# Performance work log

Hardware: AMD Instinct MI355X
Metric: run time of the kernel (lower is better)

Reference implementation:

```python
import jax, jax.numpy as jnp
import numpy as np

L, D, N_HEADS = 4096, 1024, 16
HEAD_D = D // N_HEADS


def setup_inputs() -> dict:
    key = jax.random.key(0)
    kx, kq, kbq, ko, kbo = jax.random.split(key, 5)
    lim_in = 1.0 / np.sqrt(D)
    return {
        "x": jax.random.normal(kx, (L, D), dtype=jnp.float32),
        # equinox nn.Linear(dim, 3*dim): weight [3D, D], bias [3D], uniform(-1/sqrt(in), 1/sqrt(in))
        "W_qkv": jax.random.uniform(kq, (3 * D, D), jnp.float32, -lim_in, lim_in),
        "b_qkv": jax.random.uniform(kbq, (3 * D,), jnp.float32, -lim_in, lim_in),
        "W_out": jax.random.uniform(ko, (D, D), jnp.float32, -lim_in, lim_in),
        "b_out": jax.random.uniform(kbo, (D,), jnp.float32, -lim_in, lim_in),
    }


def reference(x, W_qkv, b_qkv, W_out, b_out):
    # qkv projection: equinox Linear computes W @ x + b per token -> x @ W.T + b
    qkv = x @ W_qkv.T + b_qkv                         # [L, 3D]
    qkv = qkv.reshape(L, 3, N_HEADS, HEAD_D)
    qkv = jnp.transpose(qkv, (1, 2, 0, 3))            # [3, n, L, d]
    q, k, v = qkv[0], qkv[1], qkv[2]                  # each [n, L, d]

    scale = 1.0 / jnp.sqrt(jnp.asarray(HEAD_D, dtype=x.dtype))
    attn = jnp.einsum('nqd,nkd->nqk', q, k) * scale   # [n, L, L]
    causal = jnp.tril(jnp.ones((L, L), dtype=bool))
    attn = jnp.where(causal, attn, -jnp.inf)
    attn = jax.nn.softmax(attn, axis=-1)              # dropout rate 0 -> identity
    out = jnp.einsum('nqk,nkd->nqd', attn, v)         # [n, L, d]
    out = jnp.transpose(out, (1, 0, 2)).reshape(L, D)
    return out @ W_out.T + b_out                      # [L, D]
```

## Files before the change

kernel.cpp:

```cpp
#include <hip/hip_runtime.h>
#include <hip/hip_bf16.h>
#include <math.h>

#define L_SEQ 4096
#define DIM   1024
#define NH    16
#define HD    64

#define QSCL 0.18033688011112042f

typedef __attribute__((ext_vector_type(4)))  float f32x4;
typedef __attribute__((ext_vector_type(16))) float f32x16;
typedef __attribute__((ext_vector_type(8)))  short s16x8;
typedef __attribute__((ext_vector_type(4)))  short s16x4;
typedef __attribute__((ext_vector_type(4)))  unsigned u32x4;
typedef __attribute__((ext_vector_type(2)))  unsigned u32x2;

#if defined(__has_builtin)
#  if __has_builtin(__builtin_amdgcn_permlane32_swap)
#    define HAVE_PLSWAP 1
#  else
#    define HAVE_PLSWAP 0
#  endif
#else
#  define HAVE_PLSWAP 0
#endif

__device__ __forceinline__ short f2bf(float f) {
  unsigned u = __builtin_bit_cast(unsigned, f);
  u = u + 0x7fffu + ((u >> 16) & 1u);
  return (short)(u >> 16);
}

__device__ __forceinline__ unsigned cvt_pk_bf16(float lo, float hi_) {
  unsigned r;
  asm("v_cvt_pk_bf16_f32 %0, %1, %2" : "=v"(r) : "v"(lo), "v"(hi_));
  return r;
}

__device__ __forceinline__ float exp2_fast(float x) {
  float r;
  asm("v_exp_f32 %0, %1" : "=v"(r) : "v"(x));
  return r;
}

__device__ __forceinline__ void gload_lds16(const void* g, void* l) {
  __builtin_amdgcn_global_load_lds(
      (__attribute__((address_space(1))) void*)(g),
      (__attribute__((address_space(3))) void*)(l), 16, 0, 0);
}

#define CVT_N1 (L_SEQ * DIM / 4)
#define CVT_N2 (3 * DIM * DIM / 4)
#define CVT_N3 (DIM * DIM / 4)

__global__ __launch_bounds__(256) void cvt_all(const float* __restrict__ x,
                                               const float* __restrict__ Wqkv,
                                               const float* __restrict__ Wout,
                                               short* __restrict__ xb,
                                               short* __restrict__ wqkvb,
                                               short* __restrict__ woutb) {
  int i = blockIdx.x * 256 + threadIdx.x;
  const float* src;
  short* dst;
  int j;
  if (i < CVT_N1)               { src = x;    dst = xb;    j = i; }
  else if (i < CVT_N1 + CVT_N2) { src = Wqkv; dst = wqkvb; j = i - CVT_N1; }
  else                          { src = Wout; dst = woutb; j = i - CVT_N1 - CVT_N2; }
  f32x4 f = *(const f32x4*)(src + j * 4);
  s16x4 o;
  o[0] = f2bf(f[0]); o[1] = f2bf(f[1]); o[2] = f2bf(f[2]); o[3] = f2bf(f[3]);
  *(s16x4*)(dst + j * 4) = o;
}


#define GEMM_MAINLOOP(A_, B_, Kdim)                                            \
  f32x4 acc[4][4];                                                             \
  _Pragma("unroll") for (int m = 0; m < 4; ++m)                                \
  _Pragma("unroll") for (int n = 0; n < 4; ++n) acc[m][n] = (f32x4)0.f;        \
  const short* aptr = A_ + (bm * 128 + w * 16 + (l >> 2)) * (Kdim) + (l & 3) * 8; \
  const short* bptr = B_ + (bn * 128 + w * 16 + (l >> 2)) * (Kdim) + (l & 3) * 8; \
  short* asl = &As[(w * 16) * 32];                                             \
  short* bsl = &Bs[(w * 16) * 32];                                             \
  for (int kk = 0; kk < (Kdim); kk += 32) {                                    \
    gload_lds16(aptr + kk, asl);                                               \
    gload_lds16(aptr + kk + 64 * (Kdim), asl + 64 * 32);                       \
    gload_lds16(bptr + kk, bsl);                                               \
    gload_lds16(bptr + kk + 64 * (Kdim), bsl + 64 * 32);                       \
    __syncthreads();                                                           \
    s16x8 af[4], bfr[4];                                                       \
    _Pragma("unroll") for (int m = 0; m < 4; ++m)                              \
      af[m] = *(const s16x8*)&As[(wr * 64 + m * 16 + lr) * 32 + lg * 8];       \
    _Pragma("unroll") for (int n = 0; n < 4; ++n)                              \
      bfr[n] = *(const s16x8*)&Bs[(wc * 64 + n * 16 + lr) * 32 + lg * 8];      \
    _Pragma("unroll") for (int m = 0; m < 4; ++m)                              \
    _Pragma("unroll") for (int n = 0; n < 4; ++n)                              \
      acc[m][n] = __builtin_amdgcn_mfma_f32_16x16x32_bf16(af[m], bfr[n], acc[m][n], 0, 0, 0); \
    __syncthreads();                                                           \
  }

__global__ __launch_bounds__(256) void gemm_qkv(const short* __restrict__ A,
                                                const short* __restrict__ B,
                                                const float* __restrict__ bias,
                                                short* __restrict__ Qb,
                                                short* __restrict__ Kf,
                                                short* __restrict__ Vf) {
  __shared__ __align__(16) short As[128 * 32];
  __shared__ __align__(16) short Bs[128 * 32];
  const int t = threadIdx.x;
  const int w = t >> 6, l = t & 63;
  const int wr = w >> 1, wc = w & 1;
  const int lr = l & 15, lg = l >> 4;
  const int bid = blockIdx.x;
  const int xcd = bid & 7;
  const int ii = bid >> 3;
  const int bm = xcd * 4 + (ii & 3);
  const int bn = ii >> 2;

  GEMM_MAINLOOP(A, B, DIM)

  const int row0 = bm * 128 + wr * 64;
  const int col0 = bn * 128 + wc * 64;
#pragma unroll
  for (int n = 0; n < 4; ++n) {
    const int col = col0 + n * 16 + lr;
    const float bv = bias[col];
    const int which = col >> 10;
    const int head = (col & 1023) >> 6;
    const int d = col & 63;
    if (which == 0) {
      short* dst = Qb + (head * L_SEQ) * HD + d;
#pragma unroll
      for (int m = 0; m < 4; ++m)
#pragma unroll
        for (int j = 0; j < 4; ++j) {
          const int row = row0 + m * 16 + lg * 4 + j;
          dst[row * HD] = f2bf((acc[m][n][j] + bv) * QSCL);
        }
    } else if (which == 1) {
      const int c = d >> 4, khi = (d >> 3) & 1, e = d & 7;
      short* dst = Kf + head * (L_SEQ * HD);
#pragma unroll
      for (int m = 0; m < 4; ++m)
#pragma unroll
        for (int j = 0; j < 4; ++j) {
          const int row = row0 + m * 16 + lg * 4 + j;
          const int p = row >> 5;
          const int lane = khi * 32 + (row & 31);
          dst[((p * 4 + c) * 64 + lane) * 8 + e] = f2bf(acc[m][n][j] + bv);
        }
    } else {
      const int dh = d >> 5;
      const int dq = d & 31;
      short* dst = Vf + head * (L_SEQ * HD);
#pragma unroll
      for (int m = 0; m < 4; ++m) {
        const int rowb = row0 + m * 16 + lg * 4;
        const int tt = rowb >> 6;
        const int kc = (rowb >> 4) & 3;
        const int khi = (rowb >> 3) & 1;
        const int e0 = rowb & 7;
        s16x4 wv;
#pragma unroll
        for (int j = 0; j < 4; ++j) wv[j] = f2bf(acc[m][n][j] + bv);
        *(s16x4*)&dst[(((tt * 4 + kc) * 2 + dh) * 64 + khi * 32 + dq) * 8 + e0] = wv;
      }
    }
  }
}

__global__ __launch_bounds__(256) void gemm_out64(const short* __restrict__ A,
                                                  const short* __restrict__ B,
                                                  const float* __restrict__ bias,
                                                  float* __restrict__ C) {
  __shared__ __align__(16) short As[64 * 32];
  __shared__ __align__(16) short Bs[64 * 32];
  const int t = threadIdx.x;
  const int w = t >> 6, l = t & 63;
  const int wr = w >> 1, wc = w & 1;
  const int lr = l & 15, lg = l >> 4;
  const int bid = blockIdx.x;
  const int xcd = bid & 7;
  const int ii = bid >> 3;
  const int bm = xcd * 8 + (ii & 7);
  const int bn = ii >> 3;

  f32x4 acc[2][2];
#pragma unroll
  for (int m = 0; m < 2; ++m)
#pragma unroll
    for (int n = 0; n < 2; ++n) acc[m][n] = (f32x4)0.f;

  const short* aptr = A + (bm * 64 + (t >> 2)) * DIM + (t & 3) * 8;
  const short* bptr = B + (bn * 64 + (t >> 2)) * DIM + (t & 3) * 8;
  short* asl = &As[t * 8];
  short* bsl = &Bs[t * 8];

  for (int kk = 0; kk < DIM; kk += 32) {
    gload_lds16(aptr + kk, asl);
    gload_lds16(bptr + kk, bsl);
    __syncthreads();
    s16x8 af[2], bfr[2];
#pragma unroll
    for (int m = 0; m < 2; ++m)
      af[m] = *(const s16x8*)&As[(wr * 32 + m * 16 + lr) * 32 + lg * 8];
#pragma unroll
    for (int n = 0; n < 2; ++n)
      bfr[n] = *(const s16x8*)&Bs[(wc * 32 + n * 16 + lr) * 32 + lg * 8];
#pragma unroll
    for (int m = 0; m < 2; ++m)
#pragma unroll
      for (int n = 0; n < 2; ++n)
        acc[m][n] = __builtin_amdgcn_mfma_f32_16x16x32_bf16(af[m], bfr[n], acc[m][n], 0, 0, 0);
    __syncthreads();
  }

  const int row0 = bm * 64 + wr * 32;
  const int col0 = bn * 64 + wc * 32;
#pragma unroll
  for (int n = 0; n < 2; ++n) {
    const int col = col0 + n * 16 + lr;
    const float bv = bias[col];
#pragma unroll
    for (int m = 0; m < 2; ++m)
#pragma unroll
      for (int j = 0; j < 4; ++j) {
        const int row = row0 + m * 16 + lg * 4 + j;
        C[row * DIM + col] = acc[m][n][j] + bv;
      }
  }
}

__global__ __launch_bounds__(256, 4) void attn64(const short* __restrict__ Qb,
                                                 const short* __restrict__ Kf,
                                                 const short* __restrict__ Vf,
                                                 short* __restrict__ Ob) {
  __shared__ __align__(16) short KV[2][8192];
  const int bid = blockIdx.x;
  const int xcd = bid & 7;
  const int i = bid >> 3;
  const int head = (xcd << 1) | (i >> 6);
  const int j = i & 63;
  const int qt = (j < 32) ? (63 - j) : (j - 32);
  const int q0 = qt * 64;
  const int h = threadIdx.x >> 6;
  const int l = threadIdx.x & 63;
  const int q = l & 31;
  const int hi = l >> 5;
  const int sb = h >> 1;
  const int p = h & 1;

  const short* Qh = Qb + head * (L_SEQ * HD);
  const short* Kh = Kf + head * (L_SEQ * HD);
  const short* Vh = Vf + head * (L_SEQ * HD);
  const short* gKV = (h < 2) ? Kh : Vh;

  s16x8 qf[4];
#pragma unroll
  for (int c = 0; c < 4; ++c)
    qf[c] = *(const s16x8*)&Qh[(q0 + sb * 32 + q) * HD + c * 16 + hi * 8];

  f32x16 o0 = (f32x16)0.f, o1 = (f32x16)0.f;
  f32x4 lvec = (f32x4)0.f;

  const int nr = qt + 1;

  {
    const short* gsrc = gKV + p * 2048;
    short* lb = &KV[0][h * 2048];
#pragma unroll
    for (int c = 0; c < 4; ++c) gload_lds16(gsrc + c * 512 + l * 8, lb + c * 512);
  }
  __syncthreads();

  for (int r = 0; r < nr; ++r) {
    const int buf = r & 1;
    if (r + 1 < nr) {
      const short* gsrc = gKV + (2 * (r + 1) + p) * 2048;
      short* lb = &KV[buf ^ 1][h * 2048];
#pragma unroll
      for (int c = 0; c < 4; ++c) gload_lds16(gsrc + c * 512 + l * 8, lb + c * 512);
    }

    const bool last = (r == nr - 1);
    if (!(h == 1 && last)) {
      const short* kb = &KV[buf][p * 2048];
      const short* vb = &KV[buf][(2 + p) * 2048];

      s16x8 kfr[4];
#pragma unroll
      for (int c = 0; c < 4; ++c)
        kfr[c] = *(const s16x8*)&kb[c * 512 + l * 8];

      f32x16 s = (f32x16)0.f;
      __builtin_amdgcn_s_setprio(1);
#pragma unroll
      for (int c = 0; c < 4; ++c)
        s = __builtin_amdgcn_mfma_f32_32x32x16_bf16(kfr[c], qf[c], s, 0, 0, 0);
      __builtin_amdgcn_s_setprio(0);

      if (last && (h == 0 || h == 3)) {
        const int qrel = q - hi * 4;
#pragma unroll
        for (int rr = 0; rr < 16; ++rr) {
          const int koff = (rr & 3) + 8 * (rr >> 2);
          if (koff > qrel) s[rr] = -1e30f;
        }
      }

#pragma unroll
      for (int rr = 0; rr < 16; ++rr) s[rr] = exp2_fast(s[rr]);
#pragma unroll
      for (int rr = 0; rr < 16; ++rr) lvec[rr & 3] += s[rr];

#pragma unroll
      for (int cc = 0; cc < 2; ++cc) {
        const int roff = cc * 8;
        const unsigned A = cvt_pk_bf16(s[roff + 0], s[roff + 1]);
        const unsigned B = cvt_pk_bf16(s[roff + 2], s[roff + 3]);
        const unsigned C = cvt_pk_bf16(s[roff + 4], s[roff + 5]);
        const unsigned D = cvt_pk_bf16(s[roff + 6], s[roff + 7]);
        u32x4 pw;
#if HAVE_PLSWAP
        const u32x2 r02 = __builtin_amdgcn_permlane32_swap(A, C, false, false);
        const u32x2 r13 = __builtin_amdgcn_permlane32_swap(B, D, false, false);
        pw[0] = r02[0]; pw[1] = r13[0]; pw[2] = r02[1]; pw[3] = r13[1];
#else
        const unsigned sA = (unsigned)__shfl_xor((int)A, 32, 64);
        const unsigned sB = (unsigned)__shfl_xor((int)B, 32, 64);
        const unsigned sC = (unsigned)__shfl_xor((int)C, 32, 64);
        const unsigned sD = (unsigned)__shfl_xor((int)D, 32, 64);
        pw[0] = hi ? sC : A; pw[1] = hi ? sD : B;
        pw[2] = hi ? C : sA; pw[3] = hi ? D : sB;
#endif
        const s16x8 pf = __builtin_bit_cast(s16x8, pw);
        const s16x8 vf0 = *(const s16x8*)&vb[(cc * 2 + 0) * 512 + l * 8];
        const s16x8 vf1 = *(const s16x8*)&vb[(cc * 2 + 1) * 512 + l * 8];
        __builtin_amdgcn_s_setprio(1);
        o0 = __builtin_amdgcn_mfma_f32_32x32x16_bf16(vf0, pf, o0, 0, 0, 0);
        o1 = __builtin_amdgcn_mfma_f32_32x32x16_bf16(vf1, pf, o1, 0, 0, 0);
        __builtin_amdgcn_s_setprio(0);
      }
    }
    __syncthreads();
  }

  float lsum = (lvec[0] + lvec[1]) + (lvec[2] + lvec[3]);
  lsum += __shfl_xor(lsum, 32, 64);

  unsigned* Ms = (unsigned*)&KV[0][0];
  if (p == 1) {
    unsigned* st = Ms + (sb * 64 + l) * 17;
#pragma unroll
    for (int w2 = 0; w2 < 8; ++w2) st[w2]     = cvt_pk_bf16(o0[2 * w2], o0[2 * w2 + 1]);
#pragma unroll
    for (int w2 = 0; w2 < 8; ++w2) st[8 + w2] = cvt_pk_bf16(o1[2 * w2], o1[2 * w2 + 1]);
    st[16] = __builtin_bit_cast(unsigned, lsum);
  }
  __syncthreads();
  if (p == 0) {
    const unsigned* st = Ms + (sb * 64 + l) * 17;
    lsum += __builtin_bit_cast(float, st[16]);
#pragma unroll
    for (int w2 = 0; w2 < 8; ++w2) {
      const unsigned ua = st[w2];
      o0[2 * w2]     += __builtin_bit_cast(float, ua << 16);
      o0[2 * w2 + 1] += __builtin_bit_cast(float, ua & 0xffff0000u);
      const unsigned ub = st[8 + w2];
      o1[2 * w2]     += __builtin_bit_cast(float, ub << 16);
      o1[2 * w2 + 1] += __builtin_bit_cast(float, ub & 0xffff0000u);
    }
    const float inv = 1.f / lsum;
    const int orow = q0 + sb * 32 + q;
#pragma unroll
    for (int dh = 0; dh < 2; ++dh) {
#pragma unroll
      for (int tq = 0; tq < 4; ++tq) {
        s16x4 wv;
#pragma unroll
        for (int jj = 0; jj < 4; ++jj) {
          const int rr = tq * 4 + jj;
          const float ov = (dh == 0) ? o0[rr] : o1[rr];
          wv[jj] = f2bf(ov * inv);
        }
        *(s16x4*)&Ob[orow * DIM + head * HD + dh * 32 + tq * 8 + hi * 4] = wv;
      }
    }
  }
}

extern "C" void kernel_launch(void* const* d_in, const int* in_sizes, int n_in,
                              void* d_out, int out_size, void* d_ws, size_t ws_size,
                              hipStream_t stream) {
  const float* x    = (const float*)d_in[0];
  const float* Wqkv = (const float*)d_in[1];
  const float* bqkv = (const float*)d_in[2];
  const float* Wout = (const float*)d_in[3];
  const float* bout = (const float*)d_in[4];
  float* out = (float*)d_out;

  char* ws = (char*)d_ws;
  short* xb    = (short*)(ws);
  short* wqkvb = (short*)(ws + (8u  << 20));
  short* woutb = (short*)(ws + (14u << 20));
  short* Qb    = (short*)(ws + (16u << 20));
  short* Kf    = (short*)(ws + (24u << 20));
  short* Vf    = (short*)(ws + (32u << 20));
  short* Ob    = (short*)(ws + (40u << 20));

  cvt_all<<<(CVT_N1 + CVT_N2 + CVT_N3) / 256, 256, 0, stream>>>(x, Wqkv, Wout, xb, wqkvb, woutb);

  gemm_qkv<<<768, 256, 0, stream>>>(xb, wqkvb, bqkv, Qb, Kf, Vf);
  attn64<<<1024, 256, 0, stream>>>(Qb, Kf, Vf, Ob);
  gemm_out64<<<1024, 256, 0, stream>>>(Ob, woutb, bout, out);
}
```

Measured before the change: 125.2 us.

## Split causal attention KV range into two halves and merge partials

Each query tile's causal KV loop is now split into two halves that run as separate blocks, doubling the grid from 1024 to 2048 blocks. The aim is to improve load balance and occupancy, since long diagonal tiles otherwise dominate the tail. Each half writes an unnormalized bf16 partial output and its row sums. A new merge kernel adds the two partials and normalizes them. The cost is an extra kernel launch, extra global traffic for the partials, and some precision loss from storing unnormalized partials in bf16.

```diff
diff --git a/kernel.cpp b/kernel.cpp
--- a/kernel.cpp
+++ b/kernel.cpp
@@ -30,6 +30,10 @@
   unsigned u = __builtin_bit_cast(unsigned, f);
   u = u + 0x7fffu + ((u >> 16) & 1u);
   return (short)(u >> 16);
+}
+
+__device__ __forceinline__ float bf2f(short s) {
+  return __builtin_bit_cast(float, ((unsigned)(unsigned short)s) << 16);
 }
 
 __device__ __forceinline__ unsigned cvt_pk_bf16(float lo, float hi_) {
@@ -231,18 +235,27 @@
   }
 }
 
-__global__ __launch_bounds__(256, 4) void attn64(const short* __restrict__ Qb,
-                                                 const short* __restrict__ Kf,
-                                                 const short* __restrict__ Vf,
-                                                 short* __restrict__ Ob) {
+__global__ __launch_bounds__(256, 4) void attn64s(const short* __restrict__ Qb,
+                                                  const short* __restrict__ Kf,
+                                                  const short* __restrict__ Vf,
+                                                  short* __restrict__ Ob,
+                                                  short* __restrict__ PO1,
+                                                  float* __restrict__ LS) {
   __shared__ __align__(16) short KV[2][8192];
   const int bid = blockIdx.x;
   const int xcd = bid & 7;
   const int i = bid >> 3;
-  const int head = (xcd << 1) | (i >> 6);
-  const int j = i & 63;
-  const int qt = (j < 32) ? (63 - j) : (j - 32);
+  const int head = (xcd << 1) | (i & 1);
+  const int v = i >> 1;
+  const int g = v & 15, k = v >> 4;
+  const int half = k >> 2;
+  const int qt = ((k & 3) << 4) + ((k & 4) ? (15 - g) : g);
   const int q0 = qt * 64;
+  const int nr = qt + 1;
+  const int h1 = (qt + 2) >> 1;
+  const int r0 = half ? h1 : 0;
+  const int r1 = half ? nr : h1;
+
   const int h = threadIdx.x >> 6;
   const int l = threadIdx.x & 63;
   const int q = l & 31;
@@ -263,19 +276,17 @@
   f32x16 o0 = (f32x16)0.f, o1 = (f32x16)0.f;
   f32x4 lvec = (f32x4)0.f;
 
-  const int nr = qt + 1;
-
-  {
-    const short* gsrc = gKV + p * 2048;
-    short* lb = &KV[0][h * 2048];
+  if (r0 < r1) {
+    const short* gsrc = gKV + (2 * r0 + p) * 2048;
+    short* lb = &KV[r0 & 1][h * 2048];
 #pragma unroll
     for (int c = 0; c < 4; ++c) gload_lds16(gsrc + c * 512 + l * 8, lb + c * 512);
   }
   __syncthreads();
 
-  for (int r = 0; r < nr; ++r) {
+  for (int r = r0; r < r1; ++r) {
     const int buf = r & 1;
-    if (r + 1 < nr) {
+    if (r + 1 < r1) {
       const short* gsrc = gKV + (2 * (r + 1) + p) * 2048;
       short* lb = &KV[buf ^ 1][h * 2048];
 #pragma unroll
@@ -370,8 +381,12 @@
       o1[2 * w2]     += __builtin_bit_cast(float, ub << 16);
       o1[2 * w2 + 1] += __builtin_bit_cast(float, ub & 0xffff0000u);
     }
-    const float inv = 1.f / lsum;
-    const int orow = q0 + sb * 32 + q;
+    const int row = sb * 32 + q;
+    const int u = head * 64 + qt;
+    LS[(u * 2 + half) * 64 + row] = lsum;
+    short* dst = (half == 0)
+        ? (Ob + (q0 + row) * DIM + head * HD)
+        : (PO1 + u * 4096 + row * 64);
 #pragma unroll
     for (int dh = 0; dh < 2; ++dh) {
 #pragma unroll
@@ -380,13 +395,37 @@
 #pragma unroll
         for (int jj = 0; jj < 4; ++jj) {
           const int rr = tq * 4 + jj;
-          const float ov = (dh == 0) ? o0[rr] : o1[rr];
-          wv[jj] = f2bf(ov * inv);
+          wv[jj] = f2bf((dh == 0) ? o0[rr] : o1[rr]);
         }
-        *(s16x4*)&Ob[orow * DIM + head * HD + dh * 32 + tq * 8 + hi * 4] = wv;
+        *(s16x4*)&dst[dh * 32 + tq * 8 + hi * 4] = wv;
       }
     }
   }
+}
+
+__global__ __launch_bounds__(256) void merge_o(short* __restrict__ Ob,
+                                               const short* __restrict__ PO1,
+                                               const float* __restrict__ LS) {
+  const int u = blockIdx.x;
+  const int head = u >> 6, qt = u & 63;
+  const int t = threadIdx.x;
+  const int row = t >> 2;
+  const int cs = (t & 3) * 16;
+  const float inv = 1.f / (LS[(u * 2) * 64 + row] + LS[(u * 2 + 1) * 64 + row]);
+  short* op = Ob + (qt * 64 + row) * DIM + head * HD + cs;
+  const short* pp = PO1 + u * 4096 + row * 64 + cs;
+  s16x8 a0 = *(const s16x8*)op;
+  s16x8 a1 = *(const s16x8*)(op + 8);
+  s16x8 b0 = *(const s16x8*)pp;
+  s16x8 b1 = *(const s16x8*)(pp + 8);
+  s16x8 r0v, r1v;
+#pragma unroll
+  for (int e = 0; e < 8; ++e) {
+    r0v[e] = f2bf((bf2f(a0[e]) + bf2f(b0[e])) * inv);
+    r1v[e] = f2bf((bf2f(a1[e]) + bf2f(b1[e])) * inv);
+  }
+  *(s16x8*)op = r0v;
+  *(s16x8*)(op + 8) = r1v;
 }
 
 extern "C" void kernel_launch(void* const* d_in, const int* in_sizes, int n_in,
@@ -407,10 +446,13 @@
   short* Kf    = (short*)(ws + (24u << 20));
   short* Vf    = (short*)(ws + (32u << 20));
   short* Ob    = (short*)(ws + (40u << 20));
+  short* PO1   = (short*)(ws);
+  float* LS    = (float*)(ws + (8u << 20));
 
   cvt_all<<<(CVT_N1 + CVT_N2 + CVT_N3) / 256, 256, 0, stream>>>(x, Wqkv, Wout, xb, wqkvb, woutb);
 
   gemm_qkv<<<768, 256, 0, stream>>>(xb, wqkvb, bqkv, Qb, Kf, Vf);
-  attn64<<<1024, 256, 0, stream>>>(Qb, Kf, Vf, Ob);
+  attn64s<<<2048, 256, 0, stream>>>(Qb, Kf, Vf, Ob, PO1, LS);
+  merge_o<<<NH * 64, 256, 0, stream>>>(Ob, PO1, LS);
   gemm_out64<<<1024, 256, 0, stream>>>(Ob, woutb, bout, out);
 }
```

New measurement: 132.5 us. 5.9% more time.
